# Performance work log

Hardware: AMD Instinct MI355X
Metric: run time of the kernel (lower is better)

The kernel has to match this reference:

```python
import jax, jax.numpy as jnp
import numpy as np

NUM_PARTS = 10
COS_W = 10.0
COS_K = 100.0
EPS = 1e-6

B, V, F, VHD = 512, 6890, 13776, 20000


def setup_inputs() -> dict:
    key = jax.random.key(0)
    k1, k2, k3, k4, k5 = jax.random.split(key, 5)
    vertices = jax.random.normal(k1, (B, V, 3), dtype=jnp.float32)
    bary = jax.random.uniform(k2, (VHD, 3), dtype=jnp.float32)
    faces = jax.random.randint(k3, (F, 3), 0, V)
    hd_fid = jax.random.randint(k4, (VHD,), 0, F)
    part_fid = jax.random.randint(k5, (F,), 0, NUM_PARTS)
    return {"vertices": vertices, "bary": bary, "faces": faces,
            "hd_fid": hd_fid, "part_fid": part_fid}


def reference(vertices, bary, faces, hd_fid, part_fid):
    # --- per-part mesh volume (signed tetra volumes, segment-summed by part) ---
    tri = vertices[:, faces]                       # [B, F, 3, 3] gather face corners
    t0, t1, t2 = tri[:, :, 0], tri[:, :, 1], tri[:, :, 2]
    vol_f = jnp.einsum('bfi,bfi->bf', jnp.cross(t0, t1), t2) / 6.0   # [B, F]
    fid_onehot = jax.nn.one_hot(part_fid, NUM_PARTS, dtype=vertices.dtype)  # [F, P]
    per_part_volume = vol_f @ fid_onehot           # [B, P]

    # --- HDfy: barycentric sampling of HD vertices on faces ---
    w = bary / jnp.sum(bary, axis=-1, keepdims=True)          # barycentric weights [VHD,3]
    vidx = faces[hd_fid]                                       # [VHD, 3]
    hd_corners = vertices[:, vidx]                             # [B, VHD, 3, 3]
    vertices_hd = jnp.einsum('bvkd,vk->bvd', hd_corners, w)    # [B, VHD, 3]

    # --- per-HD-vertex part volume (bmm with one-hot == gather) ---
    hd_part = part_fid[hd_fid]                                 # [VHD]
    vol_hd = per_part_volume[:, hd_part]                       # [B, VHD]

    # --- center of mass ---
    com = jnp.sum(vertices_hd * vol_hd[..., None], axis=1) / jnp.sum(vol_hd, axis=1, keepdims=True)  # [B,3]

    # --- center of pressure via height-based pressure weights ---
    h = vertices_hd[:, :, 1]                                   # [B, VHD], ground plane at y=0
    inside = (h < 0.0).astype(vertices_hd.dtype)
    outside = (h >= 0.0).astype(vertices_hd.dtype)
    pw = inside * (1.0 - COS_K * h) + outside * jnp.exp(-COS_W * h)
    cop = jnp.sum(vertices_hd * pw[..., None], axis=1) / (jnp.sum(pw, axis=1, keepdims=True) + EPS)  # [B,3]

    # --- stability loss: xz distance between COM and COP ---
    d = com - cop
    return jnp.sqrt(d[:, 0] ** 2 + d[:, 2] ** 2)               # [B]
```

## Files before the change

kernel.cpp:

```cpp
#include <hip/hip_runtime.h>
#include <math.h>

#define NB     512
#define NV     6890
#define NF     13776
#define NVHD   20000
#define NPARTS 10
#define NTHREADS 1024
#define NWAVES (NTHREADS/64)

__global__ void build_tables(const float* __restrict__ bary,
                             const int*   __restrict__ faces,
                             const int*   __restrict__ hd_fid,
                             const int*   __restrict__ part_fid,
                             int4*  __restrict__ f_table,
                             int4*  __restrict__ hd_idx,
                             float4* __restrict__ hd_w)
{
    int i = blockIdx.x * blockDim.x + threadIdx.x;
    if (i < NF) {
        f_table[i] = make_int4(faces[3*i+0], faces[3*i+1], faces[3*i+2], part_fid[i]);
    }
    if (i < NVHD) {
        int fid = hd_fid[i];
        int i0 = faces[3*fid+0], i1 = faces[3*fid+1], i2 = faces[3*fid+2];
        int p  = part_fid[fid];
        hd_idx[i] = make_int4(i0, i1, i2, p);
        float b0 = bary[3*i+0], b1 = bary[3*i+1], b2 = bary[3*i+2];
        float inv = 1.0f / (b0 + b1 + b2);
        hd_w[i] = make_float4(b0*inv, b1*inv, b2*inv, 0.f);
    }
}

__global__ __launch_bounds__(NTHREADS) void stab_kernel(
    const float* __restrict__ vertices,
    const int4*  __restrict__ f_table,
    const int4*  __restrict__ hd_idx,
    const float4* __restrict__ hd_w,
    float*       __restrict__ out)
{
    __shared__ float4 sv[NV];
    __shared__ float  spart[NPARTS];
    __shared__ float  sredp[NWAVES][NPARTS];
    __shared__ float  sred8[NWAVES][8];

    const int tid  = threadIdx.x;
    const int b    = blockIdx.x;
    const int wave = tid >> 6;
    const int lane = tid & 63;
    const float* __restrict__ vb = vertices + (size_t)b * (NV * 3);

    for (int v = tid; v < NV; v += NTHREADS) {
        float x = vb[3 * v + 0];
        float y = vb[3 * v + 1];
        float z = vb[3 * v + 2];
        sv[v] = make_float4(x, y, z, 0.f);
    }
    __syncthreads();

    float accp[NPARTS];
    #pragma unroll
    for (int q = 0; q < NPARTS; q++) accp[q] = 0.f;

    #pragma unroll 2
    for (int f = tid; f < NF; f += NTHREADS) {
        int4 ft = f_table[f];
        float4 t0 = sv[ft.x];
        float4 t1 = sv[ft.y];
        float4 t2 = sv[ft.z];
        float cx = t0.y * t1.z - t0.z * t1.y;
        float cy = t0.z * t1.x - t0.x * t1.z;
        float cz = t0.x * t1.y - t0.y * t1.x;
        float vol = (cx * t2.x + cy * t2.y + cz * t2.z) * (1.0f / 6.0f);
        #pragma unroll
        for (int q = 0; q < NPARTS; q++) accp[q] += (ft.w == q) ? vol : 0.f;
    }
    #pragma unroll
    for (int q = 0; q < NPARTS; q++) {
        float s = accp[q];
        #pragma unroll
        for (int off = 32; off > 0; off >>= 1) s += __shfl_down(s, off, 64);
        accp[q] = s;
    }
    if (lane == 0) {
        #pragma unroll
        for (int q = 0; q < NPARTS; q++) sredp[wave][q] = accp[q];
    }
    __syncthreads();
    if (tid < NPARTS) {
        float s = 0.f;
        #pragma unroll
        for (int w = 0; w < NWAVES; w++) s += sredp[w][tid];
        spart[tid] = s;
    }
    __syncthreads();

    float sVx = 0.f, sVy = 0.f, sVz = 0.f, sVol = 0.f;
    float sPx = 0.f, sPy = 0.f, sPz = 0.f, sPw  = 0.f;

    #pragma unroll 2
    for (int v = tid; v < NVHD; v += NTHREADS) {
        int4   hi = hd_idx[v];
        float4 hw = hd_w[v];
        float4 t0 = sv[hi.x];
        float4 t1 = sv[hi.y];
        float4 t2 = sv[hi.z];
        float x = hw.x * t0.x + hw.y * t1.x + hw.z * t2.x;
        float y = hw.x * t0.y + hw.y * t1.y + hw.z * t2.y;
        float z = hw.x * t0.z + hw.y * t1.z + hw.z * t2.z;
        float vol = spart[hi.w];
        float pw  = (y < 0.f) ? fmaf(-100.f, y, 1.f) : __expf(-10.f * y);
        sVx += x * vol;  sVy += y * vol;  sVz += z * vol;  sVol += vol;
        sPx += x * pw;   sPy += y * pw;   sPz += z * pw;   sPw  += pw;
    }

    float vals[8] = {sVx, sVy, sVz, sVol, sPx, sPy, sPz, sPw};
    #pragma unroll
    for (int q = 0; q < 8; q++) {
        float s = vals[q];
        #pragma unroll
        for (int off = 32; off > 0; off >>= 1) s += __shfl_down(s, off, 64);
        vals[q] = s;
    }
    if (lane == 0) {
        #pragma unroll
        for (int q = 0; q < 8; q++) sred8[wave][q] = vals[q];
    }
    __syncthreads();
    if (tid == 0) {
        float r[8];
        #pragma unroll
        for (int q = 0; q < 8; q++) {
            float s = 0.f;
            #pragma unroll
            for (int w = 0; w < NWAVES; w++) s += sred8[w][q];
            r[q] = s;
        }
        float invVol = 1.0f / r[3];
        float invPw  = 1.0f / (r[7] + 1e-6f);
        float comx = r[0] * invVol, comz = r[2] * invVol;
        float copx = r[4] * invPw,  copz = r[6] * invPw;
        float d0 = comx - copx, d2 = comz - copz;
        out[b] = sqrtf(d0 * d0 + d2 * d2);
    }
}

extern "C" void kernel_launch(void* const* d_in, const int* in_sizes, int n_in,
                              void* d_out, int out_size, void* d_ws, size_t ws_size,
                              hipStream_t stream) {
    const float* vertices = (const float*)d_in[0];
    const float* bary     = (const float*)d_in[1];
    const int*   faces    = (const int*)d_in[2];
    const int*   hd_fid   = (const int*)d_in[3];
    const int*   part_fid = (const int*)d_in[4];
    float* out = (float*)d_out;

    char* ws = (char*)d_ws;
    int4*   f_table = (int4*)ws;
    int4*   hd_idx  = (int4*)(ws + (size_t)NF * 16);
    float4* hd_w    = (float4*)(ws + (size_t)NF * 16 + (size_t)NVHD * 16);

    build_tables<<<(NVHD + 255) / 256, 256, 0, stream>>>(bary, faces, hd_fid, part_fid,
                                                         f_table, hd_idx, hd_w);
    stab_kernel<<<NB, NTHREADS, 0, stream>>>(vertices, f_table, hd_idx, hd_w, out);
}
```

Before: 64.48 us.

## Shrink LDS footprint and pack index tables to raise block occupancy

Only the first CUT vertices are stored in LDS, split into an xy float2 array and a separate z array (12 bytes per vertex instead of 16). Vertices past CUT are read from global memory. This cuts LDS per block so that two blocks can fit per CU. Face and HD index tables are packed into 16-bit fields, and the third barycentric weight is recomputed as 1-w0-w1, which halves or more the table traffic. The costs are a branchy gather path for high-index vertices and small rounding differences in w2.

```diff
diff --git a/kernel.cpp b/kernel.cpp
--- a/kernel.cpp
+++ b/kernel.cpp
@@ -8,41 +8,41 @@
 #define NPARTS 10
 #define NTHREADS 1024
 #define NWAVES (NTHREADS/64)
+#define CUT    6698
 
 __global__ void build_tables(const float* __restrict__ bary,
                              const int*   __restrict__ faces,
                              const int*   __restrict__ hd_fid,
                              const int*   __restrict__ part_fid,
-                             int4*  __restrict__ f_table,
-                             int4*  __restrict__ hd_idx,
-                             float4* __restrict__ hd_w)
+                             uint2* __restrict__ f_pack,
+                             uint4* __restrict__ hd_pack)
 {
     int i = blockIdx.x * blockDim.x + threadIdx.x;
     if (i < NF) {
-        f_table[i] = make_int4(faces[3*i+0], faces[3*i+1], faces[3*i+2], part_fid[i]);
+        unsigned a = (unsigned)faces[3*i+0] | ((unsigned)faces[3*i+1] << 16);
+        unsigned b = (unsigned)faces[3*i+2] | ((unsigned)part_fid[i]  << 16);
+        f_pack[i] = make_uint2(a, b);
     }
     if (i < NVHD) {
         int fid = hd_fid[i];
-        int i0 = faces[3*fid+0], i1 = faces[3*fid+1], i2 = faces[3*fid+2];
-        int p  = part_fid[fid];
-        hd_idx[i] = make_int4(i0, i1, i2, p);
+        unsigned a = (unsigned)faces[3*fid+0] | ((unsigned)faces[3*fid+1] << 16);
+        unsigned b = (unsigned)faces[3*fid+2] | ((unsigned)part_fid[fid]  << 16);
         float b0 = bary[3*i+0], b1 = bary[3*i+1], b2 = bary[3*i+2];
         float inv = 1.0f / (b0 + b1 + b2);
-        hd_w[i] = make_float4(b0*inv, b1*inv, b2*inv, 0.f);
+        hd_pack[i] = make_uint4(a, b, __float_as_uint(b0*inv), __float_as_uint(b1*inv));
     }
 }
 
-__global__ __launch_bounds__(NTHREADS) void stab_kernel(
+__global__ __launch_bounds__(NTHREADS, 8) void stab_kernel(
     const float* __restrict__ vertices,
-    const int4*  __restrict__ f_table,
-    const int4*  __restrict__ hd_idx,
-    const float4* __restrict__ hd_w,
+    const uint2* __restrict__ f_pack,
+    const uint4* __restrict__ hd_pack,
     float*       __restrict__ out)
 {
-    __shared__ float4 sv[NV];
+    __shared__ float2 sxy[CUT];
+    __shared__ float  szz[CUT];
     __shared__ float  spart[NPARTS];
     __shared__ float  sredp[NWAVES][NPARTS];
-    __shared__ float  sred8[NWAVES][8];
 
     const int tid  = threadIdx.x;
     const int b    = blockIdx.x;
@@ -50,13 +50,23 @@
     const int lane = tid & 63;
     const float* __restrict__ vb = vertices + (size_t)b * (NV * 3);
 
-    for (int v = tid; v < NV; v += NTHREADS) {
+    for (int v = tid; v < CUT; v += NTHREADS) {
         float x = vb[3 * v + 0];
         float y = vb[3 * v + 1];
         float z = vb[3 * v + 2];
-        sv[v] = make_float4(x, y, z, 0.f);
+        sxy[v] = make_float2(x, y);
+        szz[v] = z;
     }
     __syncthreads();
+
+#define GETV(idx, X, Y, Z) do {                                   \
+        int _ic = (idx) < CUT ? (idx) : CUT - 1;                  \
+        float2 _t = sxy[_ic]; float _z = szz[_ic];                \
+        X = _t.x; Y = _t.y; Z = _z;                               \
+        if ((idx) >= CUT) {                                       \
+            X = vb[3*(idx)+0]; Y = vb[3*(idx)+1]; Z = vb[3*(idx)+2]; \
+        }                                                         \
+    } while (0)
 
     float accp[NPARTS];
     #pragma unroll
@@ -64,16 +74,19 @@
 
     #pragma unroll 2
     for (int f = tid; f < NF; f += NTHREADS) {
-        int4 ft = f_table[f];
-        float4 t0 = sv[ft.x];
-        float4 t1 = sv[ft.y];
-        float4 t2 = sv[ft.z];
-        float cx = t0.y * t1.z - t0.z * t1.y;
-        float cy = t0.z * t1.x - t0.x * t1.z;
-        float cz = t0.x * t1.y - t0.y * t1.x;
-        float vol = (cx * t2.x + cy * t2.y + cz * t2.z) * (1.0f / 6.0f);
+        uint2 ft = f_pack[f];
+        int i0 = ft.x & 0xFFFF, i1 = ft.x >> 16;
+        int i2 = ft.y & 0xFFFF, p  = ft.y >> 16;
+        float x0, y0, z0, x1, y1, z1, x2, y2, z2;
+        GETV(i0, x0, y0, z0);
+        GETV(i1, x1, y1, z1);
+        GETV(i2, x2, y2, z2);
+        float cx = y0 * z1 - z0 * y1;
+        float cy = z0 * x1 - x0 * z1;
+        float cz = x0 * y1 - y0 * x1;
+        float vol = (cx * x2 + cy * y2 + cz * z2) * (1.0f / 6.0f);
         #pragma unroll
-        for (int q = 0; q < NPARTS; q++) accp[q] += (ft.w == q) ? vol : 0.f;
+        for (int q = 0; q < NPARTS; q++) accp[q] += (p == q) ? vol : 0.f;
     }
     #pragma unroll
     for (int q = 0; q < NPARTS; q++) {
@@ -100,15 +113,20 @@
 
     #pragma unroll 2
     for (int v = tid; v < NVHD; v += NTHREADS) {
-        int4   hi = hd_idx[v];
-        float4 hw = hd_w[v];
-        float4 t0 = sv[hi.x];
-        float4 t1 = sv[hi.y];
-        float4 t2 = sv[hi.z];
-        float x = hw.x * t0.x + hw.y * t1.x + hw.z * t2.x;
-        float y = hw.x * t0.y + hw.y * t1.y + hw.z * t2.y;
-        float z = hw.x * t0.z + hw.y * t1.z + hw.z * t2.z;
-        float vol = spart[hi.w];
+        uint4 hp = hd_pack[v];
+        int i0 = hp.x & 0xFFFF, i1 = hp.x >> 16;
+        int i2 = hp.y & 0xFFFF, p  = hp.y >> 16;
+        float w0 = __uint_as_float(hp.z);
+        float w1 = __uint_as_float(hp.w);
+        float w2 = 1.0f - w0 - w1;
+        float x0, y0, z0, x1, y1, z1, x2, y2, z2;
+        GETV(i0, x0, y0, z0);
+        GETV(i1, x1, y1, z1);
+        GETV(i2, x2, y2, z2);
+        float x = w0 * x0 + w1 * x1 + w2 * x2;
+        float y = w0 * y0 + w1 * y1 + w2 * y2;
+        float z = w0 * z0 + w1 * z1 + w2 * z2;
+        float vol = spart[p];
         float pw  = (y < 0.f) ? fmaf(-100.f, y, 1.f) : __expf(-10.f * y);
         sVx += x * vol;  sVy += y * vol;  sVz += z * vol;  sVol += vol;
         sPx += x * pw;   sPy += y * pw;   sPz += z * pw;   sPw  += pw;
@@ -122,9 +140,10 @@
         for (int off = 32; off > 0; off >>= 1) s += __shfl_down(s, off, 64);
         vals[q] = s;
     }
+    float* sred8 = &sredp[0][0];
     if (lane == 0) {
         #pragma unroll
-        for (int q = 0; q < 8; q++) sred8[wave][q] = vals[q];
+        for (int q = 0; q < 8; q++) sred8[wave * 8 + q] = vals[q];
     }
     __syncthreads();
     if (tid == 0) {
@@ -133,7 +152,7 @@
         for (int q = 0; q < 8; q++) {
             float s = 0.f;
             #pragma unroll
-            for (int w = 0; w < NWAVES; w++) s += sred8[w][q];
+            for (int w = 0; w < NWAVES; w++) s += sred8[w * 8 + q];
             r[q] = s;
         }
         float invVol = 1.0f / r[3];
@@ -143,6 +162,7 @@
         float d0 = comx - copx, d2 = comz - copz;
         out[b] = sqrtf(d0 * d0 + d2 * d2);
     }
+#undef GETV
 }
 
 extern "C" void kernel_launch(void* const* d_in, const int* in_sizes, int n_in,
@@ -156,11 +176,10 @@
     float* out = (float*)d_out;
 
     char* ws = (char*)d_ws;
-    int4*   f_table = (int4*)ws;
-    int4*   hd_idx  = (int4*)(ws + (size_t)NF * 16);
-    float4* hd_w    = (float4*)(ws + (size_t)NF * 16 + (size_t)NVHD * 16);
+    uint2* f_pack  = (uint2*)ws;
+    uint4* hd_pack = (uint4*)(ws + (size_t)NF * 8);
 
     build_tables<<<(NVHD + 255) / 256, 256, 0, stream>>>(bary, faces, hd_fid, part_fid,
-                                                         f_table, hd_idx, hd_w);
-    stab_kernel<<<NB, NTHREADS, 0, stream>>>(vertices, f_table, hd_idx, hd_w, out);
+                                                         f_pack, hd_pack);
+    stab_kernel<<<NB, NTHREADS, 0, stream>>>(vertices, f_pack, hd_pack, out);
 }
```

Result: faster. 59.03 us (-8.4%).
